# Kernel tuning notes

Hardware: AMD Instinct MI355X
Metric: run time of the kernel (lower is better)

## Reference

```python
import jax, jax.numpy as jnp
import numpy as np

B, FIN, V, X, Y, Z = 2, 32, 768, 8, 8, 8
K, FOUT = 5, 32
NNZ = V * 8  # ~8 neighbors per vertex


def setup_inputs() -> dict:
    key = jax.random.key(0)
    k1, k2, k3, k4, k5 = jax.random.split(key, 5)
    std = np.sqrt(2.0 / (FIN * K)).astype(np.float32)
    return {
        "lap_rows": jax.random.randint(k1, (NNZ,), 0, V, dtype=jnp.int32),
        "lap_cols": jax.random.randint(k2, (NNZ,), 0, V, dtype=jnp.int32),
        "lap_vals": jax.random.normal(k3, (NNZ,), dtype=jnp.float32) * 0.1,
        "x": jax.random.normal(k4, (B, FIN, V, X, Y, Z), dtype=jnp.float32),
        "weight": jax.random.normal(k5, (K, FIN, FOUT), dtype=jnp.float32) * std,
        "bias": jnp.full((FOUT,), 0.01, dtype=jnp.float32),
    }


def reference(lap_rows, lap_cols, lap_vals, x, weight, bias):
    Bb, Fin, Vv, Xx, Yy, Zz = x.shape
    Kk, _, Fout = weight.shape

    def spmm(v):  # sparse [V,V] @ dense [V,D]
        return jax.ops.segment_sum(lap_vals[:, None] * v[lap_cols],
                                   lap_rows, num_segments=Vv)

    # [B,Fin,V,X,Y,Z] -> [V, Fin*B*X*Y*Z]
    x0 = jnp.transpose(x, (2, 1, 0, 3, 4, 5)).reshape(Vv, -1)
    xs = [x0]
    if Kk > 1:
        x1 = spmm(x0)
        xs.append(x1)
        for _ in range(2, Kk):
            x2 = 2.0 * spmm(x1) - x0
            xs.append(x2)
            x0, x1 = x1, x2
    basis = jnp.stack(xs, axis=0)  # [K, V, Fin*B*X*Y*Z]
    basis = basis.reshape(Kk, Vv, Fin, Bb, Xx, Yy, Zz)
    basis = jnp.transpose(basis, (3, 1, 4, 5, 6, 0, 2))  # [B,V,X,Y,Z,K,Fin]
    out = basis.reshape(-1, Kk * Fin) @ weight.reshape(Kk * Fin, Fout)
    out = out.reshape(Bb, Vv, Xx, Yy, Zz, Fout)
    out = jnp.transpose(out, (0, 5, 1, 2, 3, 4))  # [B,Fout,V,X,Y,Z]
    return out + bias[None, :, None, None, None, None]
```

## Files before the change

kernel.cpp:

```cpp
#include <hip/hip_runtime.h>
#include <stdint.h>

#define V      768
#define FINC   32
#define FOUTC  32
#define XYZ    512
#define NB     2
#define ROWP   40
#define MAXDEG 32
#define EROWS  (MAXDEG + 2)

typedef unsigned short u16;
typedef unsigned int   u32;
typedef short bf16x8 __attribute__((ext_vector_type(8)));
typedef float f32x4  __attribute__((ext_vector_type(4)));
typedef float f32x2  __attribute__((ext_vector_type(2)));

__device__ __forceinline__ u16 f2bf(float f) {
  u32 u = __float_as_uint(f);
  u32 r = u + 0x7fffu + ((u >> 16) & 1u);
  return (u16)(r >> 16);
}
__device__ __forceinline__ float bflo(u32 w) { return __uint_as_float(w << 16); }
__device__ __forceinline__ float bfhi(u32 w) { return __uint_as_float(w & 0xffff0000u); }
__device__ __forceinline__ u32 cvtpk_bf16(float lo, float hi) {
  u32 r;
  asm("v_cvt_pk_bf16_f32 %0, %1, %2" : "=v"(r) : "v"(lo), "v"(hi));
  return r;
}

__global__ __launch_bounds__(64) void build_ell(const int* __restrict__ rows,
                                                const int* __restrict__ cols,
                                                const float* __restrict__ vals,
                                                int nnz,
                                                int2* __restrict__ epair,
                                                int* __restrict__ deg) {
  int v = blockIdx.x;
  int lane = threadIdx.x;
  int cnt = 0;
  for (int base = 0; base < nnz; base += 64) {
    int i = base + lane;
    bool m = (i < nnz) && (rows[i] == v);
    unsigned long long mask = __ballot(m);
    if (m) {
      int pos = cnt + __popcll(mask & ((1ull << lane) - 1ull));
      if (pos < MAXDEG)
        epair[v * MAXDEG + pos] = make_int2(cols[i], __float_as_int(vals[i]));
    }
    cnt += __popcll(mask);
  }
  int d = cnt < MAXDEG ? cnt : MAXDEG;
  for (int p = d + lane; p < MAXDEG; p += 64)
    epair[v * MAXDEG + p] = make_int2(0, 0);
  if (lane == 0) deg[v] = d;
}

__global__ __launch_bounds__(V) void sort_rows(const int2* __restrict__ epair,
                                               const int* __restrict__ deg,
                                               int2* __restrict__ ep3,
                                               int* __restrict__ perm,
                                               int* __restrict__ inv_g,
                                               int* __restrict__ wtrip) {
  __shared__ int sdeg[V];
  __shared__ u16 sinv[V];
  int v = threadIdx.x;
  int d = deg[v];
  sdeg[v] = d;
  __syncthreads();
  int r = 0;
  for (int u = 0; u < V; ++u) {
    int du = sdeg[u];
    r += (du > d) || (du == d && u < v);
  }
  const unsigned long long GPK = 0x8495A6B73210ull;
  int w = (int)((GPK >> (4 * (r >> 6))) & 15ull);
  int p = w * 64 + (r & 63);
  perm[p] = v;
  inv_g[v] = p;
  sinv[v] = (u16)p;
  if ((r & 63) == 0) wtrip[w] = d;
  __syncthreads();
  for (int e = 0; e < EROWS; ++e) {
    int2 o = make_int2(0, 0);
    if (e < d) {
      int2 pe = epair[v * MAXDEG + e];
      o = make_int2((int)sinv[pe.x] * (ROWP * 2), pe.y);
    }
    ep3[e * V + p] = o;
  }
}

__global__ __launch_bounds__(512) void transpose_x(const float* __restrict__ x,
                                                   const int* __restrict__ inv_g,
                                                   u16* __restrict__ xT) {
  int g = blockIdx.x;
  int b = g / V, v = g - b * V;
  int pv = inv_g[v];
  int t = threadIdx.x;
  float vals[FINC];
  const float* src = x + ((size_t)(b * FINC) * V + v) * XYZ + t;
#pragma unroll
  for (int f = 0; f < FINC; ++f) vals[f] = src[(size_t)f * V * XYZ];
  u32 pw[16];
#pragma unroll
  for (int p = 0; p < 16; ++p)
    pw[p] = (u32)f2bf(vals[2 * p]) | ((u32)f2bf(vals[2 * p + 1]) << 16);
  uint4* dst = (uint4*)(xT + ((size_t)(b * XYZ + t) * V + pv) * FINC);
#pragma unroll
  for (int q = 0; q < 4; ++q)
    dst[q] = make_uint4(pw[4 * q], pw[4 * q + 1], pw[4 * q + 2], pw[4 * q + 3]);
}

__global__ __launch_bounds__(768, 3) void cheb_main(
    const u16* __restrict__ xT, const int2* __restrict__ ep3,
    const int* __restrict__ perm, const int* __restrict__ wtrip,
    const float* __restrict__ weight, const float* __restrict__ bias,
    u32* __restrict__ stage) {
  __shared__ __align__(16) u16   CUR[V * ROWP];
  __shared__ __align__(16) uint4 WF[5][2][64];
  __shared__ u16 PRM[V];
  __shared__ int WT[12];

  int g = blockIdx.x;
  int xcd = g & 7;
  int u = g >> 3;
  int phase = u >> 5;
  int xyz = xcd * 32 + (u & 31) + (phase & 1) * 256;
  int b = phase >> 1;
  int slice = b * XYZ + xyz;

  int tid = threadIdx.x;
  int lane = tid & 63;
  int w = tid >> 6;
  int l15 = lane & 15, l4 = lane >> 4;

  if (tid < 640) {
    int k = tid >> 7, n = (tid >> 6) & 1, ln = tid & 63;
    int a15 = ln & 15, a4 = ln >> 4;
    u32 pw[4];
#pragma unroll
    for (int p = 0; p < 4; ++p) {
      float w0 = weight[(size_t)(k * FINC + a4 * 8 + 2 * p) * FOUTC + n * 16 + a15];
      float w1 = weight[(size_t)(k * FINC + a4 * 8 + 2 * p + 1) * FOUTC + n * 16 + a15];
      pw[p] = (u32)f2bf(w0) | ((u32)f2bf(w1) << 16);
    }
    WF[k][n][ln] = make_uint4(pw[0], pw[1], pw[2], pw[3]);
  }
  if (tid < 12) WT[tid] = wtrip[tid];
  PRM[tid] = (u16)perm[tid];
  float bsv[2] = {bias[l15], bias[16 + l15]};

  u32 curpk[16], prevpk[16];
  {
    const uint4* src = (const uint4*)(xT + (size_t)slice * V * FINC) + tid * 4;
    uint4* dst = (uint4*)(CUR + tid * ROWP);
#pragma unroll
    for (int j = 0; j < 4; ++j) {
      uint4 q = src[j];
      dst[j] = q;
      curpk[4 * j] = q.x; curpk[4 * j + 1] = q.y;
      curpk[4 * j + 2] = q.z; curpk[4 * j + 3] = q.w;
    }
  }
  __syncthreads();

  int trip = __builtin_amdgcn_readfirstlane(WT[w]);
  const int2* pp = ep3 + tid;

  f32x4 acc[4][2];
#pragma unroll
  for (int a = 0; a < 4; ++a)
#pragma unroll
    for (int n = 0; n < 2; ++n) acc[a][n] = (f32x4){0.f, 0.f, 0.f, 0.f};

  auto gemm_acc = [&](int k) {
    bf16x8 bn0 = *(const bf16x8*)&WF[k][0][lane];
    bf16x8 bn1 = *(const bf16x8*)&WF[k][1][lane];
#pragma unroll
    for (int a = 0; a < 4; ++a) {
      int row = (w * 4 + a) * 16 + l15;
      bf16x8 af = *(const bf16x8*)(CUR + row * ROWP + l4 * 8);
      acc[a][0] = __builtin_amdgcn_mfma_f32_16x16x32_bf16(af, bn0, acc[a][0], 0, 0, 0);
      acc[a][1] = __builtin_amdgcn_mfma_f32_16x16x32_bf16(af, bn1, acc[a][1], 0, 0, 0);
    }
  };

  f32x2 fa2[16];
  auto gather = [&]() {
#pragma unroll
    for (int j = 0; j < 16; ++j) fa2[j] = (f32x2){0.f, 0.f};
    int2 pe0 = pp[0];
    int2 pe1 = pp[V];
    for (int e = 0; e < trip; ++e) {
      int2 nx = pp[(e + 2) * V];
      float fv = __int_as_float(pe0.y);
      f32x2 fv2 = {fv, fv};
      const uint4* sp = (const uint4*)((const char*)CUR + (u32)pe0.x);
      uint4 qa = sp[0], qb = sp[1], qc = sp[2], qd = sp[3];
      u32 wq[16] = {qa.x, qa.y, qa.z, qa.w, qb.x, qb.y, qb.z, qb.w,
                    qc.x, qc.y, qc.z, qc.w, qd.x, qd.y, qd.z, qd.w};
#pragma unroll
      for (int p = 0; p < 16; ++p) {
        f32x2 s = {bflo(wq[p]), bfhi(wq[p])};
        fa2[p] += fv2 * s;
      }
      pe0 = pe1; pe1 = nx;
    }
  };

  auto store_cur = [&]() {
    uint4* dp = (uint4*)(CUR + tid * ROWP);
#pragma unroll
    for (int j = 0; j < 4; ++j)
      dp[j] = make_uint4(curpk[4 * j], curpk[4 * j + 1], curpk[4 * j + 2], curpk[4 * j + 3]);
  };

  gemm_acc(0);
  gather();
  __syncthreads();
#pragma unroll
  for (int j = 0; j < 16; ++j) {
    prevpk[j] = curpk[j];
    curpk[j] = cvtpk_bf16(fa2[j][0], fa2[j][1]);
  }
  store_cur();
  __syncthreads();

#pragma unroll
  for (int ph = 1; ph <= 3; ++ph) {
    gemm_acc(ph);
    gather();
    __syncthreads();
#pragma unroll
    for (int j = 0; j < 16; ++j) {
      u32 pv = prevpk[j];
      float t0 = 2.f * fa2[j][0] - bflo(pv);
      float t1 = 2.f * fa2[j][1] - bfhi(pv);
      prevpk[j] = curpk[j];
      curpk[j] = cvtpk_bf16(t0, t1);
    }
    store_cur();
    __syncthreads();
  }

  gemm_acc(4);

  u32* stg = stage + (size_t)slice * (V * 16);
#pragma unroll
  for (int a = 0; a < 4; ++a) {
#pragma unroll
    for (int r = 0; r < 4; ++r) {
      int vr = PRM[(w * 4 + a) * 16 + l4 * 4 + r];
      u32 pk = cvtpk_bf16(acc[a][0][r] + bsv[0], acc[a][1][r] + bsv[1]);
      stg[vr * 16 + l15] = pk;
    }
  }
}

#define TO_VT  12
#define TO_PAD 193
__global__ __launch_bounds__(512) void transpose_out(const u32* __restrict__ stage,
                                                     float* __restrict__ out) {
  __shared__ u32 T[64 * TO_PAD];
  int g = blockIdx.x;
  int b = g >> 9, vt = (g >> 3) & 63, xt = g & 7;
  int v0 = vt * TO_VT;
  int xyz0 = xt * 64;
  int t = threadIdx.x;
  int j = t >> 3, s = t & 7;
  const u32* src = stage + (size_t)(b * XYZ + xyz0 + j) * (V * 16) + v0 * 16 + s * 24;
#pragma unroll
  for (int i = 0; i < 24; i += 4) {
    uint4 q = *(const uint4*)(src + i);
    int w0 = s * 24 + i;
    T[j * TO_PAD + w0]     = q.x;
    T[j * TO_PAD + w0 + 1] = q.y;
    T[j * TO_PAD + w0 + 2] = q.z;
    T[j * TO_PAD + w0 + 3] = q.w;
  }
  __syncthreads();
  int wv = t >> 6, lane = t & 63;
#pragma unroll
  for (int i = 0; i < 48; ++i) {
    int fout = wv * 4 + i / 12;
    int vv = i % 12;
    u32 pk = T[lane * TO_PAD + vv * 16 + (fout & 15)];
    float val = (fout < 16) ? bflo(pk) : bfhi(pk);
    out[((size_t)(b * FOUTC + fout) * V + v0 + vv) * XYZ + xyz0 + lane] = val;
  }
}

extern "C" void kernel_launch(void* const* d_in, const int* in_sizes, int n_in,
                              void* d_out, int out_size, void* d_ws, size_t ws_size,
                              hipStream_t stream) {
  const int*   lap_rows = (const int*)d_in[0];
  const int*   lap_cols = (const int*)d_in[1];
  const float* lap_vals = (const float*)d_in[2];
  const float* x        = (const float*)d_in[3];
  const float* weight   = (const float*)d_in[4];
  const float* bias     = (const float*)d_in[5];
  float* out = (float*)d_out;
  int nnz = in_sizes[0];

  char* ws = (char*)d_ws;
  const size_t XT_BYTES = (size_t)NB * XYZ * V * FINC * sizeof(u16);
  const size_t EP_BYTES = (size_t)V * MAXDEG * 8;
  const size_t E3_BYTES = (size_t)EROWS * V * 8;
  u16*  xT    = (u16*)ws;
  u32*  stg   = (u32*)ws;
  int2* epair = (int2*)(ws + XT_BYTES);
  int2* ep3   = (int2*)(ws + XT_BYTES + EP_BYTES);
  int*  deg   = (int*)(ws + XT_BYTES + EP_BYTES + E3_BYTES);
  int*  perm  = (int*)(ws + XT_BYTES + EP_BYTES + E3_BYTES + 3072);
  int*  inv_g = (int*)(ws + XT_BYTES + EP_BYTES + E3_BYTES + 6144);
  int*  wtrip = (int*)(ws + XT_BYTES + EP_BYTES + E3_BYTES + 9216);

  hipLaunchKernelGGL(build_ell, dim3(V), dim3(64), 0, stream,
                     lap_rows, lap_cols, lap_vals, nnz, epair, deg);
  hipLaunchKernelGGL(sort_rows, dim3(1), dim3(V), 0, stream,
                     epair, deg, ep3, perm, inv_g, wtrip);
  hipLaunchKernelGGL(transpose_x, dim3(NB * V), dim3(512), 0, stream, x, inv_g, xT);
  hipLaunchKernelGGL(cheb_main, dim3(NB * XYZ), dim3(768), 0, stream,
                     xT, ep3, perm, wtrip, weight, bias, stg);
  hipLaunchKernelGGL(transpose_out, dim3(NB * 64 * 8), dim3(512), 0, stream,
                     stg, out);
}
```

Before: 220.3 us.

## Spread MFMA tiles over 16 waves, unmasked bf16 high unpack, coalesced transpose loads

Grows cheb_main blocks from 768 to 1024 threads. The first 768 threads still do the sparse gather and Chebyshev recurrence, while the GEMM row tiles are now split across 16 waves at 3 tiles each instead of 12 waves at 4. The gather unpacks the high bf16 half without masking off the low bits, saving one op per element at the cost of a tiny extra rounding error. transpose_out's stage reads are rearranged so consecutive threads load consecutive 16-byte chunks. The extra waves sit idle during the gather, and the tighter launch bounds (1024, 4) may cap registers and cause spills.

```diff
diff --git a/kernel.cpp b/kernel.cpp
--- a/kernel.cpp
+++ b/kernel.cpp
@@ -23,6 +23,7 @@
 }
 __device__ __forceinline__ float bflo(u32 w) { return __uint_as_float(w << 16); }
 __device__ __forceinline__ float bfhi(u32 w) { return __uint_as_float(w & 0xffff0000u); }
+__device__ __forceinline__ float bfhi_raw(u32 w) { return __uint_as_float(w); }
 __device__ __forceinline__ u32 cvtpk_bf16(float lo, float hi) {
   u32 r;
   asm("v_cvt_pk_bf16_f32 %0, %1, %2" : "=v"(r) : "v"(lo), "v"(hi));
@@ -111,7 +112,7 @@
     dst[q] = make_uint4(pw[4 * q], pw[4 * q + 1], pw[4 * q + 2], pw[4 * q + 3]);
 }
 
-__global__ __launch_bounds__(768, 3) void cheb_main(
+__global__ __launch_bounds__(1024, 4) void cheb_main(
     const u16* __restrict__ xT, const int2* __restrict__ ep3,
     const int* __restrict__ perm, const int* __restrict__ wtrip,
     const float* __restrict__ weight, const float* __restrict__ bias,
@@ -133,6 +134,7 @@
   int lane = tid & 63;
   int w = tid >> 6;
   int l15 = lane & 15, l4 = lane >> 4;
+  bool gath = tid < V;
 
   if (tid < 640) {
     int k = tid >> 7, n = (tid >> 6) & 1, ln = tid & 63;
@@ -147,11 +149,11 @@
     WF[k][n][ln] = make_uint4(pw[0], pw[1], pw[2], pw[3]);
   }
   if (tid < 12) WT[tid] = wtrip[tid];
-  PRM[tid] = (u16)perm[tid];
+  if (gath) PRM[tid] = (u16)perm[tid];
   float bsv[2] = {bias[l15], bias[16 + l15]};
 
   u32 curpk[16], prevpk[16];
-  {
+  if (gath) {
     const uint4* src = (const uint4*)(xT + (size_t)slice * V * FINC) + tid * 4;
     uint4* dst = (uint4*)(CUR + tid * ROWP);
 #pragma unroll
@@ -164,12 +166,13 @@
   }
   __syncthreads();
 
-  int trip = __builtin_amdgcn_readfirstlane(WT[w]);
+  int trip = 0;
+  if (w < 12) trip = __builtin_amdgcn_readfirstlane(WT[w]);
   const int2* pp = ep3 + tid;
 
-  f32x4 acc[4][2];
-#pragma unroll
-  for (int a = 0; a < 4; ++a)
+  f32x4 acc[3][2];
+#pragma unroll
+  for (int a = 0; a < 3; ++a)
 #pragma unroll
     for (int n = 0; n < 2; ++n) acc[a][n] = (f32x4){0.f, 0.f, 0.f, 0.f};
 
@@ -177,8 +180,8 @@
     bf16x8 bn0 = *(const bf16x8*)&WF[k][0][lane];
     bf16x8 bn1 = *(const bf16x8*)&WF[k][1][lane];
 #pragma unroll
-    for (int a = 0; a < 4; ++a) {
-      int row = (w * 4 + a) * 16 + l15;
+    for (int a = 0; a < 3; ++a) {
+      int row = w * 48 + a * 16 + l15;
       bf16x8 af = *(const bf16x8*)(CUR + row * ROWP + l4 * 8);
       acc[a][0] = __builtin_amdgcn_mfma_f32_16x16x32_bf16(af, bn0, acc[a][0], 0, 0, 0);
       acc[a][1] = __builtin_amdgcn_mfma_f32_16x16x32_bf16(af, bn1, acc[a][1], 0, 0, 0);
@@ -201,7 +204,7 @@
                     qc.x, qc.y, qc.z, qc.w, qd.x, qd.y, qd.z, qd.w};
 #pragma unroll
       for (int p = 0; p < 16; ++p) {
-        f32x2 s = {bflo(wq[p]), bfhi(wq[p])};
+        f32x2 s = {bflo(wq[p]), bfhi_raw(wq[p])};
         fa2[p] += fv2 * s;
       }
       pe0 = pe1; pe1 = nx;
@@ -216,30 +219,34 @@
   };
 
   gemm_acc(0);
-  gather();
-  __syncthreads();
-#pragma unroll
-  for (int j = 0; j < 16; ++j) {
-    prevpk[j] = curpk[j];
-    curpk[j] = cvtpk_bf16(fa2[j][0], fa2[j][1]);
-  }
-  store_cur();
+  if (gath) gather();
+  __syncthreads();
+  if (gath) {
+#pragma unroll
+    for (int j = 0; j < 16; ++j) {
+      prevpk[j] = curpk[j];
+      curpk[j] = cvtpk_bf16(fa2[j][0], fa2[j][1]);
+    }
+    store_cur();
+  }
   __syncthreads();
 
 #pragma unroll
   for (int ph = 1; ph <= 3; ++ph) {
     gemm_acc(ph);
-    gather();
+    if (gath) gather();
     __syncthreads();
-#pragma unroll
-    for (int j = 0; j < 16; ++j) {
-      u32 pv = prevpk[j];
-      float t0 = 2.f * fa2[j][0] - bflo(pv);
-      float t1 = 2.f * fa2[j][1] - bfhi(pv);
-      prevpk[j] = curpk[j];
-      curpk[j] = cvtpk_bf16(t0, t1);
-    }
-    store_cur();
+    if (gath) {
+#pragma unroll
+      for (int j = 0; j < 16; ++j) {
+        u32 pv = prevpk[j];
+        float t0 = 2.f * fa2[j][0] - bflo(pv);
+        float t1 = 2.f * fa2[j][1] - bfhi(pv);
+        prevpk[j] = curpk[j];
+        curpk[j] = cvtpk_bf16(t0, t1);
+      }
+      store_cur();
+    }
     __syncthreads();
   }
 
@@ -247,10 +254,10 @@
 
   u32* stg = stage + (size_t)slice * (V * 16);
 #pragma unroll
-  for (int a = 0; a < 4; ++a) {
+  for (int a = 0; a < 3; ++a) {
 #pragma unroll
     for (int r = 0; r < 4; ++r) {
-      int vr = PRM[(w * 4 + a) * 16 + l4 * 4 + r];
+      int vr = PRM[w * 48 + a * 16 + l4 * 4 + r];
       u32 pk = cvtpk_bf16(acc[a][0][r] + bsv[0], acc[a][1][r] + bsv[1]);
       stg[vr * 16 + l15] = pk;
     }
@@ -267,12 +274,14 @@
   int v0 = vt * TO_VT;
   int xyz0 = xt * 64;
   int t = threadIdx.x;
-  int j = t >> 3, s = t & 7;
-  const u32* src = stage + (size_t)(b * XYZ + xyz0 + j) * (V * 16) + v0 * 16 + s * 24;
-#pragma unroll
-  for (int i = 0; i < 24; i += 4) {
-    uint4 q = *(const uint4*)(src + i);
-    int w0 = s * 24 + i;
+  const u32* base = stage + (size_t)(b * XYZ + xyz0) * (V * 16) + v0 * 16;
+#pragma unroll
+  for (int i = 0; i < 6; ++i) {
+    int idx4 = i * 512 + t;
+    int j = idx4 / 48;
+    int c4 = idx4 - j * 48;
+    uint4 q = *(const uint4*)(base + (size_t)j * (V * 16) + c4 * 4);
+    int w0 = c4 * 4;
     T[j * TO_PAD + w0]     = q.x;
     T[j * TO_PAD + w0 + 1] = q.y;
     T[j * TO_PAD + w0 + 2] = q.z;
@@ -320,7 +329,7 @@
   hipLaunchKernelGGL(sort_rows, dim3(1), dim3(V), 0, stream,
                      epair, deg, ep3, perm, inv_g, wtrip);
   hipLaunchKernelGGL(transpose_x, dim3(NB * V), dim3(512), 0, stream, x, inv_g, xT);
-  hipLaunchKernelGGL(cheb_main, dim3(NB * XYZ), dim3(768), 0, stream,
+  hipLaunchKernelGGL(cheb_main, dim3(NB * XYZ), dim3(1024), 0, stream,
                      xT, ep3, perm, wtrip, weight, bias, stg);
   hipLaunchKernelGGL(transpose_out, dim3(NB * 64 * 8), dim3(512), 0, stream,
                      stg, out);
```

Result: no change. 221.7 us (+0.6%).
